# Kernel optimization log

Hardware: AMD Instinct MI355X
Metric: run time of the kernel (lower is better)

Reference implementation:

```python
import jax, jax.numpy as jnp
import numpy as np

N = 50000   # node_count
D = 64      # dim_in (also GCN hidden, GRU hidden, top-k k)
E = 800000  # num_edges


def setup_inputs() -> dict:
    key = jax.random.key(0)
    ks = jax.random.split(key, 10)
    s = 1.0 / np.sqrt(D)
    return {
        "x": jax.random.normal(ks[0], (N, D), jnp.float32),
        "edge_index": jax.random.randint(ks[1], (2, E), 0, N, dtype=jnp.int64),
        "edge_weight": jax.random.uniform(ks[2], (E,), jnp.float32),
        # TopKPooling projection vector p
        "pool_p": jax.random.normal(ks[3], (D,), jnp.float32) * s,
        # EvolveGCNH initial weight (GRU hidden state h0), [D, D]
        "init_W": jax.random.normal(ks[4], (D, D), jnp.float32) * s,
        # GRU params, torch gate order (r, z, n)
        "gru_Wih": jax.random.normal(ks[5], (3 * D, D), jnp.float32) * s,
        "gru_Whh": jax.random.normal(ks[6], (3 * D, D), jnp.float32) * s,
        "gru_bih": jax.random.normal(ks[7], (3 * D,), jnp.float32) * s,
        "gru_bhh": jax.random.normal(ks[8], (3 * D,), jnp.float32) * s,
        # final Linear(D, 1)
        "lin_W": jax.random.normal(ks[9], (1, D), jnp.float32) * s,
        "lin_b": jnp.zeros((1,), jnp.float32),
    }


def reference(x, edge_index, edge_weight, pool_p, init_W,
              gru_Wih, gru_Whh, gru_bih, gru_bhh, lin_W, lin_b):
    n, d = x.shape
    # ---- TopKPooling: k = ceil((D/N) * N) = D nodes ----
    score = (x @ pool_p) / jnp.linalg.norm(pool_p)          # [N]
    vals, perm = jax.lax.top_k(score, d)                    # descending, k = D
    x_tilde = x[perm] * jnp.tanh(vals)[:, None]             # [D, D]
    # ---- one GRU step: batch = D pooled nodes, hidden = D, h0 = init_W ----
    gi = x_tilde @ gru_Wih.T + gru_bih                      # [D, 3D]
    gh = init_W @ gru_Whh.T + gru_bhh                       # [D, 3D]
    i_r, i_z, i_n = jnp.split(gi, 3, axis=-1)
    h_r, h_z, h_n = jnp.split(gh, 3, axis=-1)
    r = jax.nn.sigmoid(i_r + h_r)
    z = jax.nn.sigmoid(i_z + h_z)
    nn_ = jnp.tanh(i_n + r * h_n)
    W = (1.0 - z) * nn_ + z * init_W                        # evolved GCN weight [D, D]
    # ---- GCNConv_Fixed_W: add self-loops + symmetric norm + scatter ----
    loop = jnp.arange(n)
    row = jnp.concatenate([edge_index[0], loop])            # sources
    col = jnp.concatenate([edge_index[1], loop])            # targets
    w = jnp.concatenate([edge_weight, jnp.ones((n,), x.dtype)])
    deg = jax.ops.segment_sum(w, col, num_segments=n)
    deg_safe = jnp.where(deg > 0, deg, 1.0)
    dinv = jnp.where(deg > 0, jax.lax.rsqrt(deg_safe), 0.0)
    norm = dinv[row] * w * dinv[col]                        # [E+N]
    xw = x @ W                                              # [N, D]
    agg = jax.ops.segment_sum(norm[:, None] * xw[row], col, num_segments=n)
    # ---- head: relu + Linear(D, 1) ----
    h = jax.nn.relu(agg)
    return h @ lin_W.T + lin_b                              # [N, 1]
```

## Files before the change

### kernel.cpp

```cpp
#include <hip/hip_runtime.h>
#include <hip/hip_fp16.h>
#include <cmath>

#define N_NODES 50000
#define DIM 64
#define E_EDGES 800000
#define SCAN_BLOCKS 196
#define FIX 16777216.0f
#define DEG_MASK 0xFFFFFFFFFFull
#define NB_A 98
#define NRUNS 98

__global__ __launch_bounds__(256) void score_kernel(
    const float* __restrict__ x, const float* __restrict__ p,
    float* __restrict__ score, unsigned long long* __restrict__ packed,
    int* __restrict__ fillc) {
    int gid = blockIdx.x * blockDim.x + threadIdx.x;
    int n = gid >> 6, lane = gid & 63;
    if (n >= N_NODES) return;
    float pv = p[lane];
    float v = x[n * DIM + lane] * pv;
    float pn = pv * pv;
    for (int off = 32; off > 0; off >>= 1) {
        v  += __shfl_down(v, off);
        pn += __shfl_down(pn, off);
    }
    if (lane == 0) {
        score[n] = v / sqrtf(pn);
        packed[n] = (1ull << 24);
        fillc[n] = 0;
    }
}

__global__ __launch_bounds__(256) void scan1_kernel(
    const unsigned long long* __restrict__ packed,
    int* __restrict__ off, int* __restrict__ bsum, float* __restrict__ dinv) {
    __shared__ int s[256];
    int t = threadIdx.x;
    int g = blockIdx.x * 256 + t;
    unsigned long long pk = (g < N_NODES) ? packed[g] : 0ull;
    int v = (int)(pk >> 40);
    if (g < N_NODES)
        dinv[g] = rsqrtf((float)(pk & DEG_MASK) * (1.0f / FIX));
    s[t] = v;
    __syncthreads();
    for (int d = 1; d < 256; d <<= 1) {
        int add = (t >= d) ? s[t - d] : 0;
        __syncthreads();
        s[t] += add;
        __syncthreads();
    }
    if (g < N_NODES) off[g] = s[t] - v;
    if (t == 255) bsum[blockIdx.x] = s[255];
}

__global__ __launch_bounds__(256) void scan2_kernel(
    const int* __restrict__ bsum, int* __restrict__ boff) {
    __shared__ int s[256];
    int t = threadIdx.x;
    int v = (t < SCAN_BLOCKS) ? bsum[t] : 0;
    s[t] = v;
    __syncthreads();
    for (int d = 1; d < 256; d <<= 1) {
        int add = (t >= d) ? s[t - d] : 0;
        __syncthreads();
        s[t] += add;
        __syncthreads();
    }
    boff[t] = s[t] - v;
}

__global__ __launch_bounds__(256) void fill_kernel(
    const int* __restrict__ ei, const float* __restrict__ ew,
    const float* __restrict__ dinv, const int* __restrict__ off,
    const int* __restrict__ boff, int* __restrict__ fillc,
    float2* __restrict__ ren) {
    int e = blockIdx.x * blockDim.x + threadIdx.x;
    if (e >= E_EDGES) return;
    int r = ei[e], c = ei[E_EDGES + e];
    int pos = off[c] + boff[c >> 8] + atomicAdd(&fillc[c], 1);
    ren[pos] = make_float2(__int_as_float(r), dinv[r] * ew[e] * dinv[c]);
}

__device__ __forceinline__ void wave_sort64(float& v, int& idx, int lane) {
    #pragma unroll
    for (int k = 2; k <= 64; k <<= 1) {
        #pragma unroll
        for (int j = k >> 1; j > 0; j >>= 1) {
            float ov = __shfl_xor(v, j);
            int   oi = __shfl_xor(idx, j);
            bool lower = ((lane & j) == 0);
            bool up    = ((lane & k) == 0);
            bool mine_prec = (v > ov) || (v == ov && idx < oi);
            bool keep = up ? (lower == mine_prec) : (lower != mine_prec);
            if (!keep) { v = ov; idx = oi; }
        }
    }
}

__device__ __forceinline__ void wave_merge_top64(float& v, int& idx,
                                                 float bv, int bi, int lane) {
    bool a_prec = (v > bv) || (v == bv && idx < bi);
    if (!a_prec) { v = bv; idx = bi; }
    #pragma unroll
    for (int j = 32; j > 0; j >>= 1) {
        float ov = __shfl_xor(v, j);
        int   oi = __shfl_xor(idx, j);
        bool lower = ((lane & j) == 0);
        bool mine_prec = (v > ov) || (v == ov && idx < oi);
        bool keep = (lower == mine_prec);
        if (!keep) { v = ov; idx = oi; }
    }
}

__global__ __launch_bounds__(512) void topk_a_kernel(
    const float* __restrict__ score,
    float* __restrict__ cand_val, int* __restrict__ cand_idx,
    const int* __restrict__ ei, const float* __restrict__ ew,
    unsigned long long* __restrict__ packed) {
    __shared__ float sv[512];
    __shared__ int   si[512];
    int t = threadIdx.x, lane = t & 63, wv = t >> 6;
    int g = blockIdx.x * 512 + t;
    float v = (g < N_NODES) ? score[g] : -INFINITY;
    int idx = (g < N_NODES) ? g : 0x7fffffff;
    wave_sort64(v, idx, lane);
    sv[t] = v; si[t] = idx;
    __syncthreads();
    if (wv == 0) {
        #pragma unroll
        for (int r = 1; r < 8; r++)
            wave_merge_top64(v, idx, sv[r * 64 + 63 - lane], si[r * 64 + 63 - lane], lane);
        cand_val[blockIdx.x * 64 + lane] = v;
        cand_idx[blockIdx.x * 64 + lane] = idx;
    }
    for (int e = blockIdx.x * 512 + t; e < E_EDGES; e += NB_A * 512) {
        int c = ei[E_EDGES + e];
        unsigned long long q = (unsigned long long)(ew[e] * FIX);
        atomicAdd(&packed[c], (1ull << 40) | q);
    }
}

__global__ __launch_bounds__(1024) void topk_b_kernel(
    const float* __restrict__ cand_val, const int* __restrict__ cand_idx,
    const float* __restrict__ x, float* __restrict__ x_tilde) {
    __shared__ float rsv[16 * 64];
    __shared__ int   rsi[16 * 64];
    __shared__ float tval[64];
    __shared__ int   perm[64];
    int t = threadIdx.x, lane = t & 63, wv = t >> 6;
    int r0 = wv * 8;
    float v; int idx;
    if (r0 < NRUNS) { v = cand_val[r0 * 64 + lane]; idx = cand_idx[r0 * 64 + lane]; }
    else            { v = -INFINITY; idx = 0x7fffffff; }
    for (int r = r0 + 1; r < r0 + 8 && r < NRUNS; r++)
        wave_merge_top64(v, idx, cand_val[r * 64 + 63 - lane],
                         cand_idx[r * 64 + 63 - lane], lane);
    rsv[wv * 64 + lane] = v; rsi[wv * 64 + lane] = idx;
    __syncthreads();
    if (wv == 0) {
        v = rsv[lane]; idx = rsi[lane];
        for (int r = 1; r < 16; r++)
            wave_merge_top64(v, idx, rsv[r * 64 + 63 - lane],
                             rsi[r * 64 + 63 - lane], lane);
        tval[lane] = tanhf(v);
        perm[lane] = idx;
    }
    __syncthreads();
    for (int i = t; i < 4096; i += 1024) {
        int j = i >> 6, kk = i & 63;
        x_tilde[i] = x[perm[j] * DIM + kk] * tval[j];
    }
}

__global__ __launch_bounds__(64) void gru_kernel(
    const float* __restrict__ xt, const float* __restrict__ initW,
    const float* __restrict__ Wih, const float* __restrict__ Whh,
    const float* __restrict__ bih, const float* __restrict__ bhh,
    float* __restrict__ Wout) {
    __shared__ float xrow[64], hrow[64];
    int i = blockIdx.x, j = threadIdx.x;
    xrow[j] = xt[i * 64 + j];
    hrow[j] = initW[i * 64 + j];
    __syncthreads();
    float gi_r = bih[j], gi_z = bih[j + 64], gi_n = bih[j + 128];
    float gh_r = bhh[j], gh_z = bhh[j + 64], gh_n = bhh[j + 128];
    for (int k = 0; k < 64; k++) {
        float xv = xrow[k], hv = hrow[k];
        gi_r += xv * Wih[j * 64 + k];
        gi_z += xv * Wih[(j + 64) * 64 + k];
        gi_n += xv * Wih[(j + 128) * 64 + k];
        gh_r += hv * Whh[j * 64 + k];
        gh_z += hv * Whh[(j + 64) * 64 + k];
        gh_n += hv * Whh[(j + 128) * 64 + k];
    }
    float r = 1.f / (1.f + expf(-(gi_r + gh_r)));
    float z = 1.f / (1.f + expf(-(gi_z + gh_z)));
    float nn = tanhf(gi_n + r * gh_n);
    Wout[i * 64 + j] = (1.f - z) * nn + z * hrow[j];
}

__global__ __launch_bounds__(256) void xw_kernel(
    const float* __restrict__ x, const float* __restrict__ W,
    __half* __restrict__ xwh) {
    __shared__ float Wl[64 * 64];
    __shared__ float Xl[64 * 64];
    int t = threadIdx.x;
    int r0 = blockIdx.x * 64;
    for (int i = t; i < 4096; i += 256) Wl[i] = W[i];
    for (int i = t; i < 4096; i += 256) {
        int r = r0 + (i >> 6);
        Xl[i] = (r < N_NODES) ? x[r0 * 64 + i] : 0.f;
    }
    __syncthreads();
    int j = t & 63, ty = t >> 6;
    float acc[16];
    #pragma unroll
    for (int rr = 0; rr < 16; rr++) acc[rr] = 0.f;
    for (int k = 0; k < 64; k++) {
        float wvv = Wl[k * 64 + j];
        #pragma unroll
        for (int rr = 0; rr < 16; rr++)
            acc[rr] += Xl[(ty * 16 + rr) * 64 + k] * wvv;
    }
    #pragma unroll
    for (int rr = 0; rr < 16; rr++) {
        int r = r0 + ty * 16 + rr;
        if (r < N_NODES) xwh[r * DIM + j] = __float2half(acc[rr]);
    }
}

__global__ __launch_bounds__(256) void gather_head_kernel(
    const int* __restrict__ off, const int* __restrict__ boff,
    const float2* __restrict__ ren, const float* __restrict__ dinv,
    const float4* __restrict__ xwh,
    const float* __restrict__ linW, const float* __restrict__ linb,
    float* __restrict__ out) {
    int gid = blockIdx.x * blockDim.x + threadIdx.x;
    int n = gid >> 6, lane = gid & 63;
    if (n >= N_NODES) return;
    int c8 = lane & 7;
    int slot = lane >> 3;
    float acc[8];
    #pragma unroll
    for (int q = 0; q < 8; q++) acc[q] = 0.f;
    if (slot == 0) {
        float di = dinv[n];
        float s = di * di;
        float4 hv = xwh[n * 8 + c8];
        const __half2* h2 = reinterpret_cast<const __half2*>(&hv);
        #pragma unroll
        for (int q = 0; q < 4; q++) {
            float2 f = __half22float2(h2[q]);
            acc[2 * q]     = s * f.x;
            acc[2 * q + 1] = s * f.y;
        }
    }
    int s0 = off[n] + boff[n >> 8];
    int e0 = (n == N_NODES - 1) ? E_EDGES : off[n + 1] + boff[(n + 1) >> 8];
    for (int base = s0; base < e0; base += 64) {
        int m = min(64, e0 - base);
        int rv = 0; float wv = 0.f;
        if (base + lane < e0) {
            float2 pk = ren[base + lane];
            rv = __float_as_int(pk.x);
            wv = pk.y;
        }
        int G = (m + 7) >> 3;
        for (int g = 0; g < G; g++) {
            int src = g * 8 + slot;
            int r = __shfl(rv, src);
            float ww = __shfl(wv, src);
            float4 hv = xwh[r * 8 + c8];
            const __half2* h2 = reinterpret_cast<const __half2*>(&hv);
            #pragma unroll
            for (int q = 0; q < 4; q++) {
                float2 f = __half22float2(h2[q]);
                acc[2 * q]     += ww * f.x;
                acc[2 * q + 1] += ww * f.y;
            }
        }
    }
    #pragma unroll
    for (int q = 0; q < 8; q++) {
        acc[q] += __shfl_xor(acc[q], 8);
        acc[q] += __shfl_xor(acc[q], 16);
        acc[q] += __shfl_xor(acc[q], 32);
    }
    float pv = 0.f;
    #pragma unroll
    for (int q = 0; q < 8; q++)
        pv += fmaxf(acc[q], 0.f) * linW[c8 * 8 + q];
    pv += __shfl_xor(pv, 1); pv += __shfl_xor(pv, 2); pv += __shfl_xor(pv, 4);
    if (lane == 0) out[n] = pv + linb[0];
}

extern "C" void kernel_launch(void* const* d_in, const int* in_sizes, int n_in,
                              void* d_out, int out_size, void* d_ws, size_t ws_size,
                              hipStream_t stream) {
    const float* x     = (const float*)d_in[0];
    const int*   ei    = (const int*)d_in[1];
    const float* ew    = (const float*)d_in[2];
    const float* p     = (const float*)d_in[3];
    const float* initW = (const float*)d_in[4];
    const float* Wih   = (const float*)d_in[5];
    const float* Whh   = (const float*)d_in[6];
    const float* bih   = (const float*)d_in[7];
    const float* bhh   = (const float*)d_in[8];
    const float* linW  = (const float*)d_in[9];
    const float* linb  = (const float*)d_in[10];
    float* out = (float*)d_out;

    char* w = (char*)d_ws;
    unsigned long long* packed = (unsigned long long*)w; w += 8ull * N_NODES;
    float2* ren    = (float2*)w;   w += 8ull * E_EDGES;
    __half* xwh    = (__half*)w;   w += 2ull * (size_t)N_NODES * DIM;
    float* score   = (float*)w;    w += 4ull * N_NODES;
    float* dinv    = (float*)w;    w += 4ull * N_NODES;
    int*   fillc   = (int*)w;      w += 4ull * N_NODES;
    int*   off     = (int*)w;      w += 4ull * N_NODES;
    float* cand_val= (float*)w;    w += 4ull * 8192;
    int*   cand_idx= (int*)w;      w += 4ull * 8192;
    float* x_tilde = (float*)w;    w += 4ull * 4096;
    float* W       = (float*)w;    w += 4ull * 4096;
    int*   bsum    = (int*)w;      w += 4ull * 256;
    int*   boff    = (int*)w;      w += 4ull * 256;

    score_kernel<<<(N_NODES * 64 + 255) / 256, 256, 0, stream>>>(x, p, score, packed, fillc);
    topk_a_kernel<<<NB_A, 512, 0, stream>>>(score, cand_val, cand_idx, ei, ew, packed);
    topk_b_kernel<<<1, 1024, 0, stream>>>(cand_val, cand_idx, x, x_tilde);
    gru_kernel<<<64, 64, 0, stream>>>(x_tilde, initW, Wih, Whh, bih, bhh, W);
    xw_kernel<<<(N_NODES + 63) / 64, 256, 0, stream>>>(x, W, xwh);
    scan1_kernel<<<SCAN_BLOCKS, 256, 0, stream>>>(packed, off, bsum, dinv);
    scan2_kernel<<<1, 256, 0, stream>>>(bsum, boff);
    fill_kernel<<<(E_EDGES + 255) / 256, 256, 0, stream>>>(ei, ew, dinv, off, boff, fillc, ren);
    gather_head_kernel<<<(N_NODES * 64 + 255) / 256, 256, 0, stream>>>(
        off, boff, ren, dinv, (const float4*)xwh, linW, linb, out);
}
```

Baseline: 250.9 us.

## Fuse score computation into top-k stage and unroll gather loop by two

Score computation moves into the first top-k kernel, with one thread computing a node's dot product using float4 loads. This removes the score buffer round trip and the warp-per-node reduction. Zeroing of the packed and fill arrays goes to a small init kernel, and the self-loop degree is now added as +1 inside the rsqrt instead of being pre-seeded. The gather loop handles two edge groups per iteration so more loads are in flight. The per-thread strided 256-byte row reads of x are less coalesced than the old layout.

```diff
diff --git a/kernel.cpp b/kernel.cpp
--- a/kernel.cpp
+++ b/kernel.cpp
@@ -11,24 +11,80 @@
 #define NB_A 98
 #define NRUNS 98
 
-__global__ __launch_bounds__(256) void score_kernel(
+__global__ __launch_bounds__(256) void init_kernel(
+    unsigned long long* __restrict__ packed, int* __restrict__ fillc) {
+    int g = blockIdx.x * blockDim.x + threadIdx.x;
+    if (g < N_NODES) { packed[g] = 0ull; fillc[g] = 0; }
+}
+
+__device__ __forceinline__ void wave_sort64(float& v, int& idx, int lane) {
+    #pragma unroll
+    for (int k = 2; k <= 64; k <<= 1) {
+        #pragma unroll
+        for (int j = k >> 1; j > 0; j >>= 1) {
+            float ov = __shfl_xor(v, j);
+            int   oi = __shfl_xor(idx, j);
+            bool lower = ((lane & j) == 0);
+            bool up    = ((lane & k) == 0);
+            bool mine_prec = (v > ov) || (v == ov && idx < oi);
+            bool keep = up ? (lower == mine_prec) : (lower != mine_prec);
+            if (!keep) { v = ov; idx = oi; }
+        }
+    }
+}
+
+__device__ __forceinline__ void wave_merge_top64(float& v, int& idx,
+                                                 float bv, int bi, int lane) {
+    bool a_prec = (v > bv) || (v == bv && idx < bi);
+    if (!a_prec) { v = bv; idx = bi; }
+    #pragma unroll
+    for (int j = 32; j > 0; j >>= 1) {
+        float ov = __shfl_xor(v, j);
+        int   oi = __shfl_xor(idx, j);
+        bool lower = ((lane & j) == 0);
+        bool mine_prec = (v > ov) || (v == ov && idx < oi);
+        bool keep = (lower == mine_prec);
+        if (!keep) { v = ov; idx = oi; }
+    }
+}
+
+__global__ __launch_bounds__(512) void score_topk_a_kernel(
     const float* __restrict__ x, const float* __restrict__ p,
-    float* __restrict__ score, unsigned long long* __restrict__ packed,
-    int* __restrict__ fillc) {
-    int gid = blockIdx.x * blockDim.x + threadIdx.x;
-    int n = gid >> 6, lane = gid & 63;
-    if (n >= N_NODES) return;
-    float pv = p[lane];
-    float v = x[n * DIM + lane] * pv;
-    float pn = pv * pv;
-    for (int off = 32; off > 0; off >>= 1) {
-        v  += __shfl_down(v, off);
-        pn += __shfl_down(pn, off);
-    }
-    if (lane == 0) {
-        score[n] = v / sqrtf(pn);
-        packed[n] = (1ull << 24);
-        fillc[n] = 0;
+    float* __restrict__ cand_val, int* __restrict__ cand_idx,
+    const int* __restrict__ ei, const float* __restrict__ ew,
+    unsigned long long* __restrict__ packed) {
+    __shared__ float sv[512];
+    __shared__ int   si[512];
+    int t = threadIdx.x, lane = t & 63, wvid = t >> 6;
+    int g = blockIdx.x * 512 + t;
+    float v; int idx;
+    if (g < N_NODES) {
+        const float4* x4 = (const float4*)(x + (size_t)g * DIM);
+        const float4* p4 = (const float4*)p;
+        float dot = 0.f, pn = 0.f;
+        #pragma unroll
+        for (int k = 0; k < 16; k++) {
+            float4 xv = x4[k], pv = p4[k];
+            dot += xv.x * pv.x + xv.y * pv.y + xv.z * pv.z + xv.w * pv.w;
+            pn  += pv.x * pv.x + pv.y * pv.y + pv.z * pv.z + pv.w * pv.w;
+        }
+        v = dot / sqrtf(pn);
+        idx = g;
+    } else { v = -INFINITY; idx = 0x7fffffff; }
+    wave_sort64(v, idx, lane);
+    sv[t] = v; si[t] = idx;
+    __syncthreads();
+    if (wvid == 0) {
+        #pragma unroll
+        for (int r = 1; r < 8; r++)
+            wave_merge_top64(v, idx, sv[r * 64 + 63 - lane], si[r * 64 + 63 - lane], lane);
+        cand_val[blockIdx.x * 64 + lane] = v;
+        cand_idx[blockIdx.x * 64 + lane] = idx;
+    }
+    for (int e = blockIdx.x * 512 + t; e < E_EDGES; e += NB_A * 512) {
+        int c = ei[E_EDGES + e];
+        unsigned long long q = (unsigned long long)(ew[e] * FIX);
+        atomicAdd(&packed[c], (1ull << 40) | q);
     }
 }
 
@@ -41,7 +97,7 @@
     unsigned long long pk = (g < N_NODES) ? packed[g] : 0ull;
     int v = (int)(pk >> 40);
     if (g < N_NODES)
-        dinv[g] = rsqrtf((float)(pk & DEG_MASK) * (1.0f / FIX));
+        dinv[g] = rsqrtf((float)(pk & DEG_MASK) * (1.0f / FIX) + 1.0f);
     s[t] = v;
     __syncthreads();
     for (int d = 1; d < 256; d <<= 1) {
@@ -80,65 +136,6 @@
     int r = ei[e], c = ei[E_EDGES + e];
     int pos = off[c] + boff[c >> 8] + atomicAdd(&fillc[c], 1);
     ren[pos] = make_float2(__int_as_float(r), dinv[r] * ew[e] * dinv[c]);
-}
-
-__device__ __forceinline__ void wave_sort64(float& v, int& idx, int lane) {
-    #pragma unroll
-    for (int k = 2; k <= 64; k <<= 1) {
-        #pragma unroll
-        for (int j = k >> 1; j > 0; j >>= 1) {
-            float ov = __shfl_xor(v, j);
-            int   oi = __shfl_xor(idx, j);
-            bool lower = ((lane & j) == 0);
-            bool up    = ((lane & k) == 0);
-            bool mine_prec = (v > ov) || (v == ov && idx < oi);
-            bool keep = up ? (lower == mine_prec) : (lower != mine_prec);
-            if (!keep) { v = ov; idx = oi; }
-        }
-    }
-}
-
-__device__ __forceinline__ void wave_merge_top64(float& v, int& idx,
-                                                 float bv, int bi, int lane) {
-    bool a_prec = (v > bv) || (v == bv && idx < bi);
-    if (!a_prec) { v = bv; idx = bi; }
-    #pragma unroll
-    for (int j = 32; j > 0; j >>= 1) {
-        float ov = __shfl_xor(v, j);
-        int   oi = __shfl_xor(idx, j);
-        bool lower = ((lane & j) == 0);
-        bool mine_prec = (v > ov) || (v == ov && idx < oi);
-        bool keep = (lower == mine_prec);
-        if (!keep) { v = ov; idx = oi; }
-    }
-}
-
-__global__ __launch_bounds__(512) void topk_a_kernel(
-    const float* __restrict__ score,
-    float* __restrict__ cand_val, int* __restrict__ cand_idx,
-    const int* __restrict__ ei, const float* __restrict__ ew,
-    unsigned long long* __restrict__ packed) {
-    __shared__ float sv[512];
-    __shared__ int   si[512];
-    int t = threadIdx.x, lane = t & 63, wv = t >> 6;
-    int g = blockIdx.x * 512 + t;
-    float v = (g < N_NODES) ? score[g] : -INFINITY;
-    int idx = (g < N_NODES) ? g : 0x7fffffff;
-    wave_sort64(v, idx, lane);
-    sv[t] = v; si[t] = idx;
-    __syncthreads();
-    if (wv == 0) {
-        #pragma unroll
-        for (int r = 1; r < 8; r++)
-            wave_merge_top64(v, idx, sv[r * 64 + 63 - lane], si[r * 64 + 63 - lane], lane);
-        cand_val[blockIdx.x * 64 + lane] = v;
-        cand_idx[blockIdx.x * 64 + lane] = idx;
-    }
-    for (int e = blockIdx.x * 512 + t; e < E_EDGES; e += NB_A * 512) {
-        int c = ei[E_EDGES + e];
-        unsigned long long q = (unsigned long long)(ew[e] * FIX);
-        atomicAdd(&packed[c], (1ull << 40) | q);
-    }
 }
 
 __global__ __launch_bounds__(1024) void topk_b_kernel(
@@ -267,7 +264,24 @@
             wv = pk.y;
         }
         int G = (m + 7) >> 3;
-        for (int g = 0; g < G; g++) {
+        int g = 0;
+        for (; g + 2 <= G; g += 2) {
+            int src0 = g * 8 + slot, src1 = src0 + 8;
+            int   ra = __shfl(rv, src0);  float wa = __shfl(wv, src0);
+            int   rb = __shfl(rv, src1);  float wb = __shfl(wv, src1);
+            float4 ha = xwh[ra * 8 + c8];
+            float4 hb = xwh[rb * 8 + c8];
+            const __half2* h2a = reinterpret_cast<const __half2*>(&ha);
+            const __half2* h2b = reinterpret_cast<const __half2*>(&hb);
+            #pragma unroll
+            for (int q = 0; q < 4; q++) {
+                float2 fa = __half22float2(h2a[q]);
+                float2 fb = __half22float2(h2b[q]);
+                acc[2 * q]     += wa * fa.x + wb * fb.x;
+                acc[2 * q + 1] += wa * fa.y + wb * fb.y;
+            }
+        }
+        if (g < G) {
             int src = g * 8 + slot;
             int r = __shfl(rv, src);
             float ww = __shfl(wv, src);
@@ -313,11 +327,10 @@
 
     char* w = (char*)d_ws;
     unsigned long long* packed = (unsigned long long*)w; w += 8ull * N_NODES;
+    int*   fillc   = (int*)w;      w += 4ull * N_NODES;
     float2* ren    = (float2*)w;   w += 8ull * E_EDGES;
     __half* xwh    = (__half*)w;   w += 2ull * (size_t)N_NODES * DIM;
-    float* score   = (float*)w;    w += 4ull * N_NODES;
     float* dinv    = (float*)w;    w += 4ull * N_NODES;
-    int*   fillc   = (int*)w;      w += 4ull * N_NODES;
     int*   off     = (int*)w;      w += 4ull * N_NODES;
     float* cand_val= (float*)w;    w += 4ull * 8192;
     int*   cand_idx= (int*)w;      w += 4ull * 8192;
@@ -326,8 +339,8 @@
     int*   bsum    = (int*)w;      w += 4ull * 256;
     int*   boff    = (int*)w;      w += 4ull * 256;
 
-    score_kernel<<<(N_NODES * 64 + 255) / 256, 256, 0, stream>>>(x, p, score, packed, fillc);
-    topk_a_kernel<<<NB_A, 512, 0, stream>>>(score, cand_val, cand_idx, ei, ew, packed);
+    init_kernel<<<SCAN_BLOCKS, 256, 0, stream>>>(packed, fillc);
+    score_topk_a_kernel<<<NB_A, 512, 0, stream>>>(x, p, cand_val, cand_idx, ei, ew, packed);
     topk_b_kernel<<<1, 1024, 0, stream>>>(cand_val, cand_idx, x, x_tilde);
     gru_kernel<<<64, 64, 0, stream>>>(x_tilde, initW, Wih, Whh, bih, bhh, W);
     xw_kernel<<<(N_NODES + 63) / 64, 256, 0, stream>>>(x, W, xwh);
```

Result: no change. 247.8 us (-1.2%).
